# Performance work log

Measured on AMD Instinct MI355X. Metric: run time of the kernel, lower is better.

The kernel has to match this reference:

```python
import jax, jax.numpy as jnp
import numpy as np

L = 256  # hardcoded heatmap size in the original module
EPS = 1e-6
SIGMA = 1.0 / 3.0
BOX_T = 0.5
MASK_T = 0.1


def _gen_mask(Yp):
    """Faithful vectorized version of get_box_pos + make_heatmap for one [L,L] map."""
    M = jnp.where(Yp > BOX_T, Yp, 0.0)
    rows = jnp.sum(M, axis=1) > 0  # scan over rows (dim 0)
    cols = jnp.sum(M, axis=0) > 0  # scan over cols (dim 1)
    left = jnp.argmax(rows)                 # first nonzero row
    right = jnp.argmax(rows[::-1])          # offset of last nonzero row from the end
    up = jnp.argmax(cols)                   # first nonzero col
    down = jnp.argmax(cols[::-1])           # offset of last nonzero col from the end
    x_r = (right - left) // 2
    y_r = (down - up) // 2
    gt0 = (left + x_r).astype(jnp.float32)  # compared against coord0 = column index y
    gt1 = (up + y_r).astype(jnp.float32)    # compared against coord1 = row index x
    # make_heatmap: heatmap[x, y, :] = [y, x]
    ys = jnp.arange(L, dtype=jnp.float32)[None, :]  # coord0 over columns
    xs = jnp.arange(L, dtype=jnp.float32)[:, None]  # coord1 over rows
    d0 = (ys - gt0) / x_r.astype(jnp.float32)
    d1 = (xs - gt1) / y_r.astype(jnp.float32)
    h = d0 ** 4 + d1 ** 4                  # ((v^2)^2 summed over last dim)
    h = jnp.exp(-h / (2.0 * SIGMA) ** 2)
    return (h > MASK_T).astype(Yp.dtype)


def _per_sample(Yp, Yg):
    gen = _gen_mask(Yp)
    use_gt = jnp.max(Yg) > 0
    Yg_eff = jnp.where(use_gt, Yg, gen)
    positive = jnp.sum(Yg_eff * Yp)
    negative = jnp.sum((1.0 - Yg_eff) * Yp)
    return negative / (positive + EPS)


def setup_inputs() -> dict:
    key = jax.random.key(0)
    k1, k2, k3 = jax.random.split(key, 3)
    B = 512
    # predictions: background in [0, 0.4), a bright blob > 0.5 so box-finding works
    Y_pred = jax.random.uniform(k1, (B, L, L), dtype=jnp.float32) * 0.4
    blob = 0.6 + 0.4 * jax.random.uniform(k3, (B, 40, 80), dtype=jnp.float32)
    Y_pred = Y_pred.at[:, 100:140, 80:160].set(blob)
    # binary gt masks; zero out first half of batch to trigger the generated-mask branch
    Y_gt = (jax.random.uniform(k2, (B, L, L)) > 0.95).astype(jnp.float32)
    Y_gt = Y_gt.at[: B // 2].set(0.0)
    return {"Y_pred": Y_pred, "Y_gt": Y_gt}


def reference(Y_pred, Y_gt):
    ratios = jax.vmap(_per_sample)(Y_pred, Y_gt)  # [B]
    total = jnp.sum(ratios)
    N = Y_gt.shape[0]
    return jnp.where(total == 0, 0.0, jnp.log(total) / N)
```

## Files before the change

### kernel.cpp

```cpp
#include <hip/hip_runtime.h>
#include <math.h>

constexpr int L = 256;
constexpr float EPS = 1e-6f;
constexpr int SPLIT = 4;
constexpr int REC_WORDS = 20;


__device__ inline float wave_sum(float v) {
#pragma unroll
    for (int off = 32; off > 0; off >>= 1) v += __shfl_down(v, off, 64);
    return v;
}

__global__ __launch_bounds__(256) void zero_kernel(unsigned* __restrict__ w, int n) {
    const int i = blockIdx.x * 256 + threadIdx.x;
    if (i < n) w[i] = 0u;
}

__global__ __launch_bounds__(256) void pass1_kernel(
    const float* __restrict__ Yp, const float* __restrict__ Yg,
    unsigned* __restrict__ recs) {
    const int blk = blockIdx.x;
    const int b = blk >> 2;
    const int s = blk & 3;
    const int t = threadIdx.x;
    const float4* yp4 = (const float4*)(Yp + (size_t)b * L * L) + s * 4096;
    const float4* yg4 = (const float4*)(Yg + (size_t)b * L * L) + s * 4096;
    unsigned* rec = recs + b * REC_WORDS;

    __shared__ unsigned rowmask[8], colmask[8];
    __shared__ float part1[4], part2[4];
    if (t < 8) { rowmask[t] = 0u; colmask[t] = 0u; }
    __syncthreads();

    float sum_p = 0.f, sum_pg = 0.f;
    int anyg = 0;
#pragma unroll 4
    for (int k = 0; k < 16; ++k) {
        const int j = t + (k << 8);
        const float4 p = yp4[j];
        const float4 g = yg4[j];
        sum_p  += (p.x + p.y) + (p.z + p.w);
        sum_pg += p.x * g.x + p.y * g.y + p.z * g.z + p.w * g.w;
        anyg |= (g.x > 0.f) | (g.y > 0.f) | (g.z > 0.f) | (g.w > 0.f);
        const bool bx = p.x > 0.5f, by = p.y > 0.5f,
                   bz = p.z > 0.5f, bw = p.w > 0.5f;
        if (bx | by | bz | bw) {
            const int gj = s * 4096 + j;
            const int row = gj >> 6;
            atomicOr(&rowmask[row >> 5], 1u << (row & 31));
            const int c0 = (gj << 2) & 255;
            const unsigned bits =
                ((unsigned)bx | ((unsigned)by << 1) | ((unsigned)bz << 2) |
                 ((unsigned)bw << 3)) << (c0 & 31);
            atomicOr(&colmask[c0 >> 5], bits);
        }
    }
    const int wave = t >> 6, lane = t & 63;
    const int wany = __any(anyg);
    if (lane == 0 && wany) atomicOr(&rec[2], 1u);

    float w1 = wave_sum(sum_p);
    float w2 = wave_sum(sum_pg);
    if (lane == 0) { part1[wave] = w1; part2[wave] = w2; }
    __syncthreads();

    if (t == 0) {
        atomicAdd((float*)&rec[0], part1[0] + part1[1] + part1[2] + part1[3]);
        atomicAdd((float*)&rec[1], part2[0] + part2[1] + part2[2] + part2[3]);
    } else if (t >= 32 && t < 40) {
        const unsigned m = rowmask[t - 32];
        if (m) atomicOr(&rec[3 + (t - 32)], m);
    } else if (t >= 40 && t < 48) {
        const unsigned m = colmask[t - 40];
        if (m) atomicOr(&rec[11 + (t - 40)], m);
    }
}

__global__ __launch_bounds__(64) void pass2_kernel(
    const float* __restrict__ Yp, const unsigned* __restrict__ recs,
    float* __restrict__ ratios) {
    const int b = blockIdx.x;
    const int lane = threadIdx.x;
    const unsigned* rec = recs + b * REC_WORDS;
    const float* yp = Yp + (size_t)b * L * L;

    const float sum_p  = ((const float*)rec)[0];
    const float sum_pg = ((const float*)rec)[1];
    const unsigned anyg = rec[2];

    int first_r = 0, last_r = 0, first_c = 0, last_c = 0;
    bool any_r = false, any_c = false;
#pragma unroll
    for (int i = 0; i < 8; ++i) {
        const unsigned wr = rec[3 + i];
        if (wr) {
            if (!any_r) { first_r = i * 32 + __builtin_ffs((int)wr) - 1; any_r = true; }
            last_r = i * 32 + 31 - __builtin_clz(wr);
        }
        const unsigned wc = rec[11 + i];
        if (wc) {
            if (!any_c) { first_c = i * 32 + __builtin_ffs((int)wc) - 1; any_c = true; }
            last_c = i * 32 + 31 - __builtin_clz(wc);
        }
    }
    const int left  = any_r ? first_r : 0;
    const int right = any_r ? (L - 1 - last_r) : 0;
    const int up    = any_c ? first_c : 0;
    const int down  = any_c ? (L - 1 - last_c) : 0;
    const int x_r = (right - left) >> 1;
    const int y_r = (down - up) >> 1;
    const float gt0 = (float)(left + x_r);
    const float gt1 = (float)(up + y_r);

    float positive;
    if (anyg) {
        positive = sum_pg;
    } else if (x_r == 0 || y_r == 0) {
        positive = 0.f;
    } else {
        const float inv_xr = 1.f / (float)x_r;
        const float inv_yr = 1.f / (float)y_r;
        const float mx = fabsf((float)x_r) * 1.02f + 1.f;
        const float my = fabsf((float)y_r) * 1.02f + 1.f;
        const int cl = max(0, (int)floorf(gt0 - mx));
        const int ch = min(L - 1, (int)ceilf(gt0 + mx));
        const int rl = max(0, (int)floorf(gt1 - my));
        const int rh = min(L - 1, (int)ceilf(gt1 + my));
        const int W = ch - cl + 1, H = rh - rl + 1;
        float pos = 0.f;
        for (int idx = lane; idx < W * H; idx += 64) {
            const int r = rl + idx / W;
            const int c = cl + idx % W;
            float d0 = ((float)c - gt0) * inv_xr;
            float d1 = ((float)r - gt1) * inv_yr;
            d0 *= d0; d0 *= d0;
            d1 *= d1; d1 *= d1;
            const float h = __expf(-2.25f * (d0 + d1));
            if (h > 0.1f) pos += yp[r * L + c];
        }
        positive = wave_sum(pos);
    }
    if (lane == 0) ratios[b] = (sum_p - positive) / (positive + EPS);
}

__global__ __launch_bounds__(256) void finalize_kernel(
    const float* __restrict__ ratios, float* __restrict__ out, int B) {
    float v = 0.f;
    for (int i = threadIdx.x; i < B; i += 256) v += ratios[i];
    v = wave_sum(v);
    __shared__ float part[4];
    const int wave = threadIdx.x >> 6, lane = threadIdx.x & 63;
    if (lane == 0) part[wave] = v;
    __syncthreads();
    if (threadIdx.x == 0) {
        const float total = part[0] + part[1] + part[2] + part[3];
        out[0] = (total == 0.f) ? 0.f : logf(total) / (float)B;
    }
}

extern "C" void kernel_launch(void* const* d_in, const int* in_sizes, int n_in,
                              void* d_out, int out_size, void* d_ws, size_t ws_size,
                              hipStream_t stream) {
    const float* Yp = (const float*)d_in[0];
    const float* Yg = (const float*)d_in[1];
    const int B = in_sizes[0] / (L * L);
    unsigned* recs = (unsigned*)d_ws;
    float* ratios = (float*)((char*)d_ws + (size_t)B * REC_WORDS * 4);
    const int nz = B * REC_WORDS;
    zero_kernel<<<(nz + 255) / 256, 256, 0, stream>>>(recs, nz);
    pass1_kernel<<<B * SPLIT, 256, 0, stream>>>(Yp, Yg, recs);
    pass2_kernel<<<B, 64, 0, stream>>>(Yp, recs, ratios);
    finalize_kernel<<<1, 256, 0, stream>>>(ratios, (float*)d_out, B);
}
```

Before: 285.2 us.

## Replace bitmask atomics with min/max bbox reduction and preload all loads

Splits each sample over 8 blocks instead of 4 and issues all 16 float4 loads per thread up front to raise memory-level parallelism. Replaces the per-element shared-memory atomicOr row/column bitmasks with per-thread bbox tracking, reduced by wave and block min/max and then global atomicMin/atomicMax, which cuts the record from 20 words to 8. Pass2 then reads the bbox directly instead of scanning bitmasks. The cost is higher register pressure from the preloaded arrays and a more involved init of sentinel values.

```diff
diff --git a/kernel.cpp b/kernel.cpp
--- a/kernel.cpp
+++ b/kernel.cpp
@@ -3,8 +3,8 @@
 
 constexpr int L = 256;
 constexpr float EPS = 1e-6f;
-constexpr int SPLIT = 4;
-constexpr int REC_WORDS = 20;
+constexpr int SPLIT = 8;
+constexpr int REC_WORDS = 8;
 
 
 __device__ inline float wave_sum(float v) {
@@ -12,69 +12,104 @@
     for (int off = 32; off > 0; off >>= 1) v += __shfl_down(v, off, 64);
     return v;
 }
+__device__ inline int wave_min(int v) {
+#pragma unroll
+    for (int off = 32; off > 0; off >>= 1) v = min(v, __shfl_down(v, off, 64));
+    return v;
+}
+__device__ inline int wave_max(int v) {
+#pragma unroll
+    for (int off = 32; off > 0; off >>= 1) v = max(v, __shfl_down(v, off, 64));
+    return v;
+}
 
-__global__ __launch_bounds__(256) void zero_kernel(unsigned* __restrict__ w, int n) {
+__global__ __launch_bounds__(256) void init_kernel(unsigned* __restrict__ w, int n) {
     const int i = blockIdx.x * 256 + threadIdx.x;
-    if (i < n) w[i] = 0u;
+    if (i < n) {
+        const int k = i & 7;
+        unsigned v = 0u;
+        if (k == 3 || k == 5) v = 0x7FFFFFFFu;
+        else if (k == 4 || k == 6) v = 0xFFFFFFFFu;
+        w[i] = v;
+    }
 }
 
 __global__ __launch_bounds__(256) void pass1_kernel(
     const float* __restrict__ Yp, const float* __restrict__ Yg,
     unsigned* __restrict__ recs) {
-    const int blk = blockIdx.x;
-    const int b = blk >> 2;
-    const int s = blk & 3;
+    const int b = blockIdx.x >> 3;
+    const int s = blockIdx.x & 7;
     const int t = threadIdx.x;
-    const float4* yp4 = (const float4*)(Yp + (size_t)b * L * L) + s * 4096;
-    const float4* yg4 = (const float4*)(Yg + (size_t)b * L * L) + s * 4096;
+    const float4* yp4 = (const float4*)(Yp + (size_t)b * L * L) + s * 2048;
+    const float4* yg4 = (const float4*)(Yg + (size_t)b * L * L) + s * 2048;
     unsigned* rec = recs + b * REC_WORDS;
 
-    __shared__ unsigned rowmask[8], colmask[8];
-    __shared__ float part1[4], part2[4];
-    if (t < 8) { rowmask[t] = 0u; colmask[t] = 0u; }
-    __syncthreads();
+    float4 P[8], G[8];
+#pragma unroll
+    for (int k = 0; k < 8; ++k) P[k] = yp4[t + (k << 8)];
+#pragma unroll
+    for (int k = 0; k < 8; ++k) G[k] = yg4[t + (k << 8)];
+
+    const int rowbase = s * 32 + (t >> 6);
+    const int c0 = (t & 63) << 2;
 
     float sum_p = 0.f, sum_pg = 0.f;
     int anyg = 0;
-#pragma unroll 4
-    for (int k = 0; k < 16; ++k) {
-        const int j = t + (k << 8);
-        const float4 p = yp4[j];
-        const float4 g = yg4[j];
+    unsigned rowbits = 0u;
+    unsigned cb0 = 0, cb1 = 0, cb2 = 0, cb3 = 0;
+#pragma unroll
+    for (int k = 0; k < 8; ++k) {
+        const float4 p = P[k], g = G[k];
         sum_p  += (p.x + p.y) + (p.z + p.w);
         sum_pg += p.x * g.x + p.y * g.y + p.z * g.z + p.w * g.w;
         anyg |= (g.x > 0.f) | (g.y > 0.f) | (g.z > 0.f) | (g.w > 0.f);
-        const bool bx = p.x > 0.5f, by = p.y > 0.5f,
-                   bz = p.z > 0.5f, bw = p.w > 0.5f;
-        if (bx | by | bz | bw) {
-            const int gj = s * 4096 + j;
-            const int row = gj >> 6;
-            atomicOr(&rowmask[row >> 5], 1u << (row & 31));
-            const int c0 = (gj << 2) & 255;
-            const unsigned bits =
-                ((unsigned)bx | ((unsigned)by << 1) | ((unsigned)bz << 2) |
-                 ((unsigned)bw << 3)) << (c0 & 31);
-            atomicOr(&colmask[c0 >> 5], bits);
+        const unsigned bx = p.x > 0.5f, by = p.y > 0.5f,
+                       bz = p.z > 0.5f, bw = p.w > 0.5f;
+        rowbits |= (bx | by | bz | bw) << k;
+        cb0 |= bx; cb1 |= by; cb2 |= bz; cb3 |= bw;
+    }
+    int minr = 0x7FFFFFFF, maxr = -1, minc = 0x7FFFFFFF, maxc = -1;
+    if (rowbits) {
+        minr = rowbase + 4 * __builtin_ctz(rowbits);
+        maxr = rowbase + 4 * (31 - __builtin_clz(rowbits));
+        const unsigned colbits = cb0 | (cb1 << 1) | (cb2 << 2) | (cb3 << 3);
+        minc = c0 + __builtin_ctz(colbits);
+        maxc = c0 + (31 - __builtin_clz(colbits));
+    }
+
+    const int wave = t >> 6, lane = t & 63;
+    const float wsp = wave_sum(sum_p);
+    const float wspg = wave_sum(sum_pg);
+    const int wanyg = __any(anyg);
+    const int wminr = wave_min(minr), wmaxr = wave_max(maxr);
+    const int wminc = wave_min(minc), wmaxc = wave_max(maxc);
+
+    __shared__ float sh_p[4], sh_pg[4];
+    __shared__ int sh_a[4], sh_minr[4], sh_maxr[4], sh_minc[4], sh_maxc[4];
+    if (lane == 0) {
+        sh_p[wave] = wsp; sh_pg[wave] = wspg; sh_a[wave] = wanyg;
+        sh_minr[wave] = wminr; sh_maxr[wave] = wmaxr;
+        sh_minc[wave] = wminc; sh_maxc[wave] = wmaxc;
+    }
+    __syncthreads();
+    if (t == 0) {
+        float sp = 0.f, spg = 0.f;
+        int a = 0, mnr = 0x7FFFFFFF, mxr = -1, mnc = 0x7FFFFFFF, mxc = -1;
+#pragma unroll
+        for (int i = 0; i < 4; ++i) {
+            sp += sh_p[i]; spg += sh_pg[i]; a |= sh_a[i];
+            mnr = min(mnr, sh_minr[i]); mxr = max(mxr, sh_maxr[i]);
+            mnc = min(mnc, sh_minc[i]); mxc = max(mxc, sh_maxc[i]);
         }
-    }
-    const int wave = t >> 6, lane = t & 63;
-    const int wany = __any(anyg);
-    if (lane == 0 && wany) atomicOr(&rec[2], 1u);
-
-    float w1 = wave_sum(sum_p);
-    float w2 = wave_sum(sum_pg);
-    if (lane == 0) { part1[wave] = w1; part2[wave] = w2; }
-    __syncthreads();
-
-    if (t == 0) {
-        atomicAdd((float*)&rec[0], part1[0] + part1[1] + part1[2] + part1[3]);
-        atomicAdd((float*)&rec[1], part2[0] + part2[1] + part2[2] + part2[3]);
-    } else if (t >= 32 && t < 40) {
-        const unsigned m = rowmask[t - 32];
-        if (m) atomicOr(&rec[3 + (t - 32)], m);
-    } else if (t >= 40 && t < 48) {
-        const unsigned m = colmask[t - 40];
-        if (m) atomicOr(&rec[11 + (t - 40)], m);
+        atomicAdd((float*)&rec[0], sp);
+        atomicAdd((float*)&rec[1], spg);
+        if (a) atomicOr(&rec[2], 1u);
+        if (mxr >= 0) {
+            atomicMin((int*)&rec[3], mnr);
+            atomicMax((int*)&rec[4], mxr);
+            atomicMin((int*)&rec[5], mnc);
+            atomicMax((int*)&rec[6], mxc);
+        }
     }
 }
 
@@ -89,26 +124,14 @@
     const float sum_p  = ((const float*)rec)[0];
     const float sum_pg = ((const float*)rec)[1];
     const unsigned anyg = rec[2];
+    const int minr = (int)rec[3], maxr = (int)rec[4];
+    const int minc = (int)rec[5], maxc = (int)rec[6];
 
-    int first_r = 0, last_r = 0, first_c = 0, last_c = 0;
-    bool any_r = false, any_c = false;
-#pragma unroll
-    for (int i = 0; i < 8; ++i) {
-        const unsigned wr = rec[3 + i];
-        if (wr) {
-            if (!any_r) { first_r = i * 32 + __builtin_ffs((int)wr) - 1; any_r = true; }
-            last_r = i * 32 + 31 - __builtin_clz(wr);
-        }
-        const unsigned wc = rec[11 + i];
-        if (wc) {
-            if (!any_c) { first_c = i * 32 + __builtin_ffs((int)wc) - 1; any_c = true; }
-            last_c = i * 32 + 31 - __builtin_clz(wc);
-        }
-    }
-    const int left  = any_r ? first_r : 0;
-    const int right = any_r ? (L - 1 - last_r) : 0;
-    const int up    = any_c ? first_c : 0;
-    const int down  = any_c ? (L - 1 - last_c) : 0;
+    const bool any_r = maxr >= 0, any_c = maxc >= 0;
+    const int left  = any_r ? minr : 0;
+    const int right = any_r ? (L - 1 - maxr) : 0;
+    const int up    = any_c ? minc : 0;
+    const int down  = any_c ? (L - 1 - maxc) : 0;
     const int x_r = (right - left) >> 1;
     const int y_r = (down - up) >> 1;
     const float gt0 = (float)(left + x_r);
@@ -169,7 +192,7 @@
     unsigned* recs = (unsigned*)d_ws;
     float* ratios = (float*)((char*)d_ws + (size_t)B * REC_WORDS * 4);
     const int nz = B * REC_WORDS;
-    zero_kernel<<<(nz + 255) / 256, 256, 0, stream>>>(recs, nz);
+    init_kernel<<<(nz + 255) / 256, 256, 0, stream>>>(recs, nz);
     pass1_kernel<<<B * SPLIT, 256, 0, stream>>>(Yp, Yg, recs);
     pass2_kernel<<<B, 64, 0, stream>>>(Yp, recs, ratios);
     finalize_kernel<<<1, 256, 0, stream>>>(ratios, (float*)d_out, B);
```

Measured after the change: 279.2 us. 1.02x faster.
